# Performance work log

Measured on AMD Instinct MI355X. Metric: run time of the kernel, lower is better.

## Reference

```python
import jax, jax.numpy as jnp
import numpy as np

B, S, DIM, H = 2, 2048, 1024, 16
HD = DIM // H  # 64


def setup_inputs() -> dict:
    key = jax.random.key(0)
    ks = jax.random.split(key, 7)
    sc = 1.0 / np.sqrt(DIM)
    gammas = jnp.asarray(1.0 - 2.0 ** (-5.0 - np.arange(H)), jnp.float32)  # RetNet per-head decay
    return {
        "q": jax.random.normal(ks[0], (B, S, DIM), jnp.float32),
        "k": jax.random.normal(ks[1], (B, S, DIM), jnp.float32),
        "v": jax.random.normal(ks[2], (B, S, DIM), jnp.float32),
        "W_in": jax.random.normal(ks[3], (DIM, DIM), jnp.float32) * sc,
        "b_in": jnp.zeros((DIM,), jnp.float32),
        "W_gate": jax.random.normal(ks[4], (DIM, DIM), jnp.float32) * sc,
        "b_gate": jnp.zeros((DIM,), jnp.float32),
        "W_out": jax.random.normal(ks[5], (DIM, DIM), jnp.float32) * sc,
        "b_out": jnp.zeros((DIM,), jnp.float32),
        "gammas": gammas,
    }


def _mamba(x, W_in, b_in, W_gate, b_gate, W_out, b_out):
    # Gated linear recurrence: h_t = a_t * h_{t-1} + u_t  (selective-scan style)
    u = x @ W_in + b_in          # [B,S,D]
    a = jax.nn.sigmoid(x @ W_gate + b_gate)  # [B,S,D] data-dependent decay gate

    def combine(c1, c2):
        a1, u1 = c1
        a2, u2 = c2
        return (a1 * a2, a2 * u1 + u2)

    _, h = jax.lax.associative_scan(combine, (a, u), axis=1)  # parallel scan over S
    return h @ W_out + b_out  # residual=False, dropout=0.0


def _retention(q, k, v, gammas):
    # Per-head decay-masked attention: out = ((Q K^T / sqrt(hd)) * D) V,
    # D[h,n,m] = gamma_h^(n-m) for n>=m else 0 (causal decay kernel).
    def split(x):
        return x.reshape(B, S, H, HD).transpose(0, 2, 1, 3)  # [B,H,S,HD]

    qh, kh, vh = split(q), split(k), split(v)
    idx = jnp.arange(S)
    diff = idx[:, None] - idx[None, :]                        # [S,S]
    expnt = jnp.maximum(diff, 0).astype(jnp.float32)
    D = jnp.where(diff >= 0, gammas[:, None, None] ** expnt, 0.0)  # [H,S,S]
    scores = jnp.einsum("bhnd,bhmd->bhnm", qh, kh) / np.sqrt(HD)
    out = jnp.einsum("bhnm,bhmd->bhnd", scores * D[None], vh)
    return out.transpose(0, 2, 1, 3).reshape(B, S, DIM)


def reference(q, k, v, W_in, b_in, W_gate, b_gate, W_out, b_out, gammas):
    q_proj = _mamba(q, W_in, b_in, W_gate, b_gate, W_out, b_out)
    return _retention(q_proj, k, v, gammas)
```

## Files before the change

kernel.cpp:

```cpp
#include <hip/hip_runtime.h>
#include <math.h>

#define B_  2
#define S_  2048
#define D_  1024
#define H_  16
#define HD_ 64
#define M_  (B_*S_)

typedef unsigned short ushort_t;
typedef unsigned int   uint_t;
typedef __attribute__((ext_vector_type(8))) short bf16x8;
typedef __attribute__((ext_vector_type(4))) float f32x4;

__device__ __forceinline__ ushort_t f2bf(float f) {
    uint_t u = __builtin_bit_cast(uint_t, f);
    u += 0x7FFFu + ((u >> 16) & 1u);
    return (ushort_t)(u >> 16);
}
__device__ __forceinline__ float bf2f(ushort_t h) {
    uint_t u = (uint_t)h << 16;
    return __builtin_bit_cast(float, u);
}
__device__ __forceinline__ uint_t pkt(float lo, float hi) {
    return __builtin_amdgcn_perm(__builtin_bit_cast(uint_t, hi),
                                 __builtin_bit_cast(uint_t, lo), 0x07060302u);
}
__device__ __forceinline__ void dma16(const ushort_t* g, ushort_t* l) {
    __builtin_amdgcn_global_load_lds(
        (const __attribute__((address_space(1))) uint_t*)g,
        (__attribute__((address_space(3))) uint_t*)l, 16, 0, 0);
}
__device__ __forceinline__ bf16x8 fragr(const ushort_t* base, int row, int chunk) {
    return *(const bf16x8*)&base[row * 64 + (((chunk ^ (row & 7)) << 3))];
}
__device__ __forceinline__ bf16x8 fragr32(const ushort_t* base, int row, int chunk) {
    return *(const bf16x8*)&base[row * 32 + (((chunk ^ ((row >> 1) & 3)) << 3))];
}

__global__ __launch_bounds__(256)
void transp_cvt3(const float* __restrict__ W0, const float* __restrict__ W1,
                 const float* __restrict__ W2, ushort_t* __restrict__ T0,
                 ushort_t* __restrict__ T1, ushort_t* __restrict__ T2) {
    __shared__ float T[32][36];
    const float*  W  = (blockIdx.z == 0) ? W0 : (blockIdx.z == 1) ? W1 : W2;
    ushort_t*     WT = (blockIdx.z == 0) ? T0 : (blockIdx.z == 1) ? T1 : T2;
    const int kt = blockIdx.x, nt = blockIdx.y;
    const int t = threadIdx.x;
    const int rr = t >> 3, cc = (t & 7) * 4;
    float4 w4 = *(const float4*)(W + (size_t)(kt * 32 + rr) * D_ + nt * 32 + cc);
    T[rr][cc + 0] = w4.x; T[rr][cc + 1] = w4.y; T[rr][cc + 2] = w4.z; T[rr][cc + 3] = w4.w;
    __syncthreads();
    ushort_t o[4];
    #pragma unroll
    for (int j = 0; j < 4; ++j) o[j] = f2bf(T[cc + j][rr]);
    *(ushort4*)(WT + (size_t)(nt * 32 + rr) * D_ + kt * 32 + cc) =
        make_ushort4(o[0], o[1], o[2], o[3]);
}

__global__ __launch_bounds__(256)
void cvt_bf16(const float* __restrict__ X, ushort_t* __restrict__ Y) {
    const int i = (blockIdx.x * 256 + threadIdx.x) * 4;
    float4 x = *(const float4*)(X + i);
    *(ushort4*)(Y + i) = make_ushort4(f2bf(x.x), f2bf(x.y), f2bf(x.z), f2bf(x.w));
}

__global__ __launch_bounds__(256)
void kv_cvt_g(const float* __restrict__ K, const float* __restrict__ V,
              const float* __restrict__ gammas, ushort_t* __restrict__ Kb,
              ushort_t* __restrict__ VT, float* __restrict__ Gg) {
    __shared__ ushort_t Tv[64 * 72];
    __shared__ ushort_t Tk[64 * 72];
    const int mt = blockIdx.x, h = blockIdx.y, b = blockIdx.z;
    const int m0 = mt * 64;
    const int tid = threadIdx.x;
    const int r = tid >> 2, c0 = (tid & 3) * 16;
    const float lg = log2f(gammas[h]);
    const float gm = exp2f(-(float)r * lg);
    {
        const float* src = K + ((size_t)(b * S_ + m0 + r)) * D_ + h * HD_ + c0;
        ushort_t kb[16];
        #pragma unroll
        for (int j4 = 0; j4 < 4; ++j4) {
            float4 x = *(const float4*)(src + j4 * 4);
            kb[j4 * 4 + 0] = f2bf(x.x); kb[j4 * 4 + 1] = f2bf(x.y);
            kb[j4 * 4 + 2] = f2bf(x.z); kb[j4 * 4 + 3] = f2bf(x.w);
        }
        ushort_t* dst = Kb + ((size_t)(b * S_ + m0 + r)) * D_ + h * HD_ + c0;
        *(uint4*)(dst + 0) = *(const uint4*)&kb[0];
        *(uint4*)(dst + 8) = *(const uint4*)&kb[8];
        #pragma unroll
        for (int j = 0; j < 16; ++j) Tk[(c0 + j) * 72 + r] = kb[j];
    }
    {
        const float* src = V + ((size_t)(b * S_ + m0 + r)) * D_ + h * HD_ + c0;
        #pragma unroll
        for (int j4 = 0; j4 < 4; ++j4) {
            float4 x = *(const float4*)(src + j4 * 4);
            Tv[(c0 + j4 * 4 + 0) * 72 + r] = f2bf(x.x * gm);
            Tv[(c0 + j4 * 4 + 1) * 72 + r] = f2bf(x.y * gm);
            Tv[(c0 + j4 * 4 + 2) * 72 + r] = f2bf(x.z * gm);
            Tv[(c0 + j4 * 4 + 3) * 72 + r] = f2bf(x.w * gm);
        }
    }
    __syncthreads();
    {
        ushort_t* dst = VT + ((size_t)((b * H_ + h) * HD_ + r)) * S_ + m0 + c0;
        *(uint4*)(dst + 0) = *(const uint4*)&Tv[r * 72 + c0 + 0];
        *(uint4*)(dst + 8) = *(const uint4*)&Tv[r * 72 + c0 + 8];
    }
    const int w = tid >> 6, lane = tid & 63, quad = lane >> 4, l15 = lane & 15;
    bf16x8 af0 = *(const bf16x8*)&Tv[(w * 16 + l15) * 72 + quad * 8];
    bf16x8 af1 = *(const bf16x8*)&Tv[(w * 16 + l15) * 72 + 32 + quad * 8];
    float* gout = Gg + ((size_t)((b * H_ + h) * 32 + mt)) * 4096;
    #pragma unroll
    for (int kt2 = 0; kt2 < 4; ++kt2) {
        bf16x8 bf0 = *(const bf16x8*)&Tk[(kt2 * 16 + l15) * 72 + quad * 8];
        bf16x8 bf1 = *(const bf16x8*)&Tk[(kt2 * 16 + l15) * 72 + 32 + quad * 8];
        f32x4 g = {};
        g = __builtin_amdgcn_mfma_f32_16x16x32_bf16(af0, bf0, g, 0, 0, 0);
        g = __builtin_amdgcn_mfma_f32_16x16x32_bf16(af1, bf1, g, 0, 0, 0);
        #pragma unroll
        for (int reg = 0; reg < 4; ++reg)
            gout[(w * 16 + quad * 4 + reg) * 64 + kt2 * 16 + l15] = g[reg];
    }
}

__global__ __launch_bounds__(256)
void gemm_dual_scan(const ushort_t* __restrict__ A, const ushort_t* __restrict__ BTi,
                    const ushort_t* __restrict__ BTg, const float* __restrict__ bi,
                    const float* __restrict__ bg, float* __restrict__ Hloc,
                    ushort_t* __restrict__ Pp, float* __restrict__ cA,
                    float* __restrict__ cU) {
    __shared__ ushort_t smem[32768];
    const int tid = threadIdx.x;
    const int n0 = blockIdx.x * 64, m0 = blockIdx.y * 128;
    const int w = tid >> 6, lane = tid & 63, quad = lane >> 4, l15 = lane & 15;
    const int wr = (w >> 1) * 64, wc = (w & 1) * 32;
    const int l4 = lane & 3, lr4 = lane >> 2;

    f32x4 acc_i[4][2] = {};
    f32x4 acc_g[4][2] = {};

    auto stage = [&](int k0, int bufo) {
        #pragma unroll
        for (int t = 0; t < 2; ++t) {
            const int row = w * 32 + t * 16 + lr4;
            const int gc = ((l4 ^ ((row >> 1) & 3)) << 3);
            dma16(A + (size_t)(m0 + row) * D_ + k0 + gc, &smem[bufo + row * 32 + l4 * 8]);
        }
        {
            const int row = w * 16 + lr4;
            const int gc = ((l4 ^ ((row >> 1) & 3)) << 3);
            dma16(BTi + (size_t)(n0 + row) * D_ + k0 + gc, &smem[bufo + 4096 + row * 32 + l4 * 8]);
            dma16(BTg + (size_t)(n0 + row) * D_ + k0 + gc, &smem[bufo + 6144 + row * 32 + l4 * 8]);
        }
    };

    stage(0, 0);
    stage(32, 8192);
    stage(64, 16384);
    for (int t = 0; t < 32; ++t) {
        if (t < 30)       asm volatile("s_waitcnt vmcnt(8)" ::: "memory");
        else if (t == 30) asm volatile("s_waitcnt vmcnt(4)" ::: "memory");
        else              asm volatile("s_waitcnt vmcnt(0)" ::: "memory");
        __builtin_amdgcn_s_barrier();
        if (t < 29) stage((t + 3) * 32, ((t + 3) & 3) * 8192);
        const ushort_t* As = smem + (t & 3) * 8192;
        const ushort_t* Bi_ = As + 4096;
        const ushort_t* Bg_ = As + 6144;
        bf16x8 af[4], bfi[2], bfg[2];
        #pragma unroll
        for (int i = 0; i < 4; ++i)
            af[i] = fragr32(As, wr + 16 * i + l15, quad);
        #pragma unroll
        for (int j = 0; j < 2; ++j) {
            bfi[j] = fragr32(Bi_, wc + 16 * j + l15, quad);
            bfg[j] = fragr32(Bg_, wc + 16 * j + l15, quad);
        }
        __builtin_amdgcn_s_setprio(1);
        #pragma unroll
        for (int i = 0; i < 4; ++i)
            #pragma unroll
            for (int j = 0; j < 2; ++j) {
                acc_i[i][j] = __builtin_amdgcn_mfma_f32_16x16x32_bf16(
                    af[i], bfi[j], acc_i[i][j], 0, 0, 0);
                acc_g[i][j] = __builtin_amdgcn_mfma_f32_16x16x32_bf16(
                    af[i], bfg[j], acc_g[i][j], 0, 0, 0);
            }
        __builtin_amdgcn_s_setprio(0);
    }

    ushort_t* Us = smem;
    ushort_t* Gu = smem + 8448;
    #pragma unroll
    for (int j = 0; j < 2; ++j) {
        const int n = wc + 16 * j + l15;
        const float bbi = bi[n0 + n], bbg = bg[n0 + n];
        #pragma unroll
        for (int i = 0; i < 4; ++i) {
            #pragma unroll
            for (int r = 0; r < 4; ++r) {
                const int m = wr + 16 * i + quad * 4 + r;
                Us[m * 66 + n] = f2bf(acc_i[i][j][r] + bbi);
                float g = 1.0f / (1.0f + __expf(-(acc_g[i][j][r] + bbg)));
                Gu[m * 66 + n] = (ushort_t)__float2uint_rn(g * 65535.0f);
            }
        }
    }
    __syncthreads();

    const int nl = tid & 63, c = tid >> 6;
    const int gmb = m0 + c * 32;
    const size_t gbase = (size_t)gmb * D_ + n0 + nl;
    float Aa = 1.0f, hh = 0.0f;
    #pragma unroll 4
    for (int j = 0; j < 32; ++j) {
        const float g = (float)Gu[(c * 32 + j) * 66 + nl] * (1.0f / 65535.0f);
        const float u = bf2f(Us[(c * 32 + j) * 66 + nl]);
        Aa *= g;
        hh = fmaf(g, hh, u);
        Pp[gbase + (size_t)j * D_] = f2bf(Aa);
        Hloc[gbase + (size_t)j * D_] = hh;
    }
    const int bb = gmb >> 11;
    const int ch = (gmb & 2047) >> 5;
    const int ci = ((bb * 64 + ch) << 10) + n0 + nl;
    cA[ci] = Aa;
    cU[ci] = hh;
}

__global__ __launch_bounds__(256)
void mid_scan(const float* __restrict__ Gg, const float* __restrict__ gammas,
              ushort_t* __restrict__ Sb, const float* __restrict__ cA,
              const float* __restrict__ cU, float* __restrict__ cIn) {
    const int bi = blockIdx.x;
    if (bi < 128) {
        const int sl = bi & 3, h = (bi >> 2) & 15, b = bi >> 6;
        const float g64 = exp2f(64.0f * log2f(gammas[h]));
        const int r = threadIdx.x >> 4;
        const int cb = (threadIdx.x & 15) * 4;
        const size_t base = ((size_t)((b * H_ + h) * 32)) * 4096 + (sl * 16 + r) * 64 + cb;
        float4 S = make_float4(0.f, 0.f, 0.f, 0.f);
        for (int c = 0; c < 32; ++c) {
            ushort4 sb;
            sb.x = f2bf(S.x); sb.y = f2bf(S.y); sb.z = f2bf(S.z); sb.w = f2bf(S.w);
            *(ushort4*)(Sb + base + (size_t)c * 4096) = sb;
            float4 G = *(const float4*)(Gg + base + (size_t)c * 4096);
            S.x = g64 * (S.x + G.x); S.y = g64 * (S.y + G.y);
            S.z = g64 * (S.z + G.z); S.w = g64 * (S.w + G.w);
        }
        return;
    }
    const int t = (bi - 128) * 256 + threadIdx.x;
    const int d = t & 1023, b = t >> 10;
    float h = 0.0f;
    for (int c0 = 0; c0 < 64; c0 += 16) {
        float Av[16], Uv[16];
        #pragma unroll
        for (int j = 0; j < 16; ++j) {
            const int idx = ((b * 64 + c0 + j) << 10) + d;
            Av[j] = cA[idx]; Uv[j] = cU[idx];
        }
        #pragma unroll
        for (int j = 0; j < 16; ++j) {
            cIn[((b * 64 + c0 + j) << 10) + d] = h;
            h = fmaf(Av[j], h, Uv[j]);
        }
    }
}

__global__ __launch_bounds__(256)
void scan_fix(const float* __restrict__ Hloc, const ushort_t* __restrict__ Pp,
              const float* __restrict__ cIn, ushort_t* __restrict__ hout) {
    const int i = (blockIdx.x * 256 + threadIdx.x) * 4;
    const int m = i >> 10, d = i & 1023;
    const int b = m >> 11, ch = (m & 2047) >> 5;
    float4 hl = *(const float4*)(Hloc + i);
    ushort4 p4 = *(const ushort4*)(Pp + i);
    float4 ci = *(const float4*)(cIn + ((b * 64 + ch) << 10) + d);
    ushort4 o;
    o.x = f2bf(fmaf(ci.x, bf2f(p4.x), hl.x));
    o.y = f2bf(fmaf(ci.y, bf2f(p4.y), hl.y));
    o.z = f2bf(fmaf(ci.z, bf2f(p4.z), hl.z));
    o.w = f2bf(fmaf(ci.w, bf2f(p4.w), hl.w));
    *(ushort4*)(hout + i) = o;
}

__global__ __launch_bounds__(256)
void gemm_out_a(const ushort_t* __restrict__ A, const ushort_t* __restrict__ BT,
                const float* __restrict__ bias, float scale,
                ushort_t* __restrict__ Cb) {
    __shared__ ushort_t smem[24576];
    const int tid = threadIdx.x;
    const int n0 = blockIdx.x * 64, m0 = blockIdx.y * 128;
    const int w = tid >> 6, lane = tid & 63, quad = lane >> 4, l15 = lane & 15;
    const int wr = (w >> 1) * 64, wc = (w & 1) * 32;
    const int l4 = lane & 3, lr4 = lane >> 2;

    f32x4 acc[4][2] = {};

    auto stage = [&](int k0, int bufo) {
        #pragma unroll
        for (int t = 0; t < 2; ++t) {
            const int row = w * 32 + t * 16 + lr4;
            const int gc = ((l4 ^ ((row >> 1) & 3)) << 3);
            dma16(A + (size_t)(m0 + row) * D_ + k0 + gc, &smem[bufo + row * 32 + l4 * 8]);
        }
        {
            const int row = w * 16 + lr4;
            const int gc = ((l4 ^ ((row >> 1) & 3)) << 3);
            dma16(BT + (size_t)(n0 + row) * D_ + k0 + gc, &smem[bufo + 4096 + row * 32 + l4 * 8]);
        }
    };

    stage(0, 0);
    stage(32, 6144);
    stage(64, 12288);
    for (int t = 0; t < 32; ++t) {
        if (t < 30)       asm volatile("s_waitcnt vmcnt(6)" ::: "memory");
        else if (t == 30) asm volatile("s_waitcnt vmcnt(3)" ::: "memory");
        else              asm volatile("s_waitcnt vmcnt(0)" ::: "memory");
        __builtin_amdgcn_s_barrier();
        if (t < 29) stage((t + 3) * 32, ((t + 3) & 3) * 6144);
        const ushort_t* As = smem + (t & 3) * 6144;
        const ushort_t* Bs = As + 4096;
        bf16x8 af[4], bf[2];
        #pragma unroll
        for (int i = 0; i < 4; ++i)
            af[i] = fragr32(As, wr + 16 * i + l15, quad);
        #pragma unroll
        for (int j = 0; j < 2; ++j)
            bf[j] = fragr32(Bs, wc + 16 * j + l15, quad);
        __builtin_amdgcn_s_setprio(1);
        #pragma unroll
        for (int i = 0; i < 4; ++i)
            #pragma unroll
            for (int j = 0; j < 2; ++j)
                acc[i][j] = __builtin_amdgcn_mfma_f32_16x16x32_bf16(
                    af[i], bf[j], acc[i][j], 0, 0, 0);
        __builtin_amdgcn_s_setprio(0);
    }

    #pragma unroll
    for (int j = 0; j < 2; ++j) {
        const int n = n0 + wc + 16 * j + l15;
        const float bb = bias[n];
        #pragma unroll
        for (int i = 0; i < 4; ++i)
            #pragma unroll
            for (int r = 0; r < 4; ++r) {
                const int m = m0 + wr + 16 * i + quad * 4 + r;
                Cb[(size_t)m * D_ + n] = f2bf((acc[i][j][r] + bb) * scale);
            }
    }
}

__global__ __launch_bounds__(256)
void retention_chunk(const ushort_t* __restrict__ Qb, const ushort_t* __restrict__ Kb,
                     const ushort_t* __restrict__ VT, const ushort_t* __restrict__ Sb,
                     const float* __restrict__ gammas, float* __restrict__ Out) {
    __shared__ ushort_t smem[20480];
    ushort_t* Qs = smem;
    ushort_t* Ks = smem + 4096;
    ushort_t* Vt = smem + 8192;
    ushort_t* Ss = smem + 12288;
    ushort_t* Ps = smem + 16384;
    const int tid = threadIdx.x;
    const int nt = blockIdx.x, h = blockIdx.y, b = blockIdx.z;
    const int n0 = nt * 64;
    const float lg = log2f(gammas[h]);
    const int w = tid >> 6, lane = tid & 63, quad = lane >> 4, l15 = lane & 15;
    const int l8 = lane & 7, lr8 = lane >> 3;
    const int nl = w * 16 + l15;
    const size_t bS = (size_t)b * S_;
    const size_t vrow0 = (size_t)((b * H_ + h) * HD_);
    const size_t sbase = ((size_t)((b * H_ + h) * 32 + nt)) * 4096;

    #pragma unroll
    for (int t = 0; t < 2; ++t) {
        const int row = w * 16 + t * 8 + lr8;
        const int gc = ((l8 ^ (row & 7)) << 3);
        dma16(Qb + (bS + n0 + row) * D_ + h * HD_ + gc, &Qs[row * 64 + l8 * 8]);
        dma16(Kb + (bS + n0 + row) * D_ + h * HD_ + gc, &Ks[row * 64 + l8 * 8]);
        dma16(VT + (vrow0 + row) * S_ + n0 + gc, &Vt[row * 64 + l8 * 8]);
        dma16(Sb + sbase + (size_t)row * 64 + gc, &Ss[row * 64 + l8 * 8]);
    }
    __syncthreads();

    bf16x8 qf0 = fragr(Qs, nl, quad);
    bf16x8 qf1 = fragr(Qs, nl, 4 + quad);

    f32x4 o[4] = {};
    #pragma unroll
    for (int ct = 0; ct < 4; ++ct) {
        bf16x8 sf0 = fragr(Ss, ct * 16 + l15, quad);
        bf16x8 sf1 = fragr(Ss, ct * 16 + l15, 4 + quad);
        o[ct] = __builtin_amdgcn_mfma_f32_16x16x32_bf16(sf0, qf0, o[ct], 0, 0, 0);
        o[ct] = __builtin_amdgcn_mfma_f32_16x16x32_bf16(sf1, qf1, o[ct], 0, 0, 0);
    }
    #pragma unroll
    for (int mt2 = 0; mt2 < 4; ++mt2) {
        bf16x8 kf0 = fragr(Ks, mt2 * 16 + l15, quad);
        bf16x8 kf1 = fragr(Ks, mt2 * 16 + l15, 4 + quad);
        f32x4 s = {};
        s = __builtin_amdgcn_mfma_f32_16x16x32_bf16(kf0, qf0, s, 0, 0, 0);
        s = __builtin_amdgcn_mfma_f32_16x16x32_bf16(kf1, qf1, s, 0, 0, 0);
        const int mbase = mt2 * 16 + quad * 4;
        #pragma unroll
        for (int r = 0; r < 4; ++r)
            if (nl < mbase + r) s[r] = 0.0f;
        uint2 pw; pw.x = pkt(s[0], s[1]); pw.y = pkt(s[2], s[3]);
        const int chunk = mbase >> 3;
        *(uint2*)&Ps[nl * 64 + ((chunk ^ (nl & 7)) << 3) + (mbase & 7)] = pw;
    }
    bf16x8 pf0 = fragr(Ps, nl, quad);
    bf16x8 pf1 = fragr(Ps, nl, 4 + quad);
    #pragma unroll
    for (int ct = 0; ct < 4; ++ct) {
        bf16x8 vf0 = fragr(Vt, ct * 16 + l15, quad);
        bf16x8 vf1 = fragr(Vt, ct * 16 + l15, 4 + quad);
        o[ct] = __builtin_amdgcn_mfma_f32_16x16x32_bf16(vf0, pf0, o[ct], 0, 0, 0);
        o[ct] = __builtin_amdgcn_mfma_f32_16x16x32_bf16(vf1, pf1, o[ct], 0, 0, 0);
    }

    const float esc = exp2f((float)nl * lg);
    const size_t ob = (bS + n0 + nl) * D_ + h * HD_;
    #pragma unroll
    for (int ct = 0; ct < 4; ++ct) {
        f32x4 t = o[ct] * esc;
        *(f32x4*)(Out + ob + ct * 16 + quad * 4) = t;
    }
}

extern "C" void kernel_launch(void* const* d_in, const int* in_sizes, int n_in,
                              void* d_out, int out_size, void* d_ws, size_t ws_size,
                              hipStream_t stream) {
    const float* q      = (const float*)d_in[0];
    const float* k      = (const float*)d_in[1];
    const float* v      = (const float*)d_in[2];
    const float* W_in   = (const float*)d_in[3];
    const float* b_in   = (const float*)d_in[4];
    const float* W_gate = (const float*)d_in[5];
    const float* b_gate = (const float*)d_in[6];
    const float* W_out  = (const float*)d_in[7];
    const float* b_out  = (const float*)d_in[8];
    const float* gammas = (const float*)d_in[9];
    float* out = (float*)d_out;

    char* ws = (char*)d_ws;
    const size_t MB = 1024 * 1024;
    float*    Hloc    = (float*)(ws);
    ushort_t* Pp      = (ushort_t*)(ws + 16 * MB);
    ushort_t* h_bf    = (ushort_t*)(ws + 24 * MB);
    ushort_t* q_bf    = (ushort_t*)(ws + 32 * MB);
    ushort_t* WT_in   = (ushort_t*)(ws + 40 * MB);
    ushort_t* WT_gate = (ushort_t*)(ws + 42 * MB);
    ushort_t* WT_out  = (ushort_t*)(ws + 44 * MB);
    float*    cA      = (float*)(ws + 46 * MB);
    float*    cU      = (float*)(ws + 46 * MB + 512 * 1024);
    float*    cIn     = (float*)(ws + 47 * MB);
    ushort_t* k_bf    = (ushort_t*)(ws + 48 * MB);
    ushort_t* VT      = (ushort_t*)(ws + 56 * MB);
    float*    Gg      = (float*)(ws + 64 * MB);
    ushort_t* Sb      = (ushort_t*)(ws + 80 * MB);
    ushort_t* qp_bf   = q_bf;

    transp_cvt3<<<dim3(D_ / 32, D_ / 32, 3), 256, 0, stream>>>(
        W_in, W_gate, W_out, WT_in, WT_gate, WT_out);
    cvt_bf16<<<(M_ * D_) / (256 * 4), 256, 0, stream>>>(q, q_bf);

    gemm_dual_scan<<<dim3(D_ / 64, M_ / 128), 256, 0, stream>>>(
        q_bf, WT_in, WT_gate, b_in, b_gate, Hloc, Pp, cA, cU);

    kv_cvt_g<<<dim3(S_ / 64, H_, B_), 256, 0, stream>>>(k, v, gammas, k_bf, VT, Gg);

    mid_scan<<<136, 256, 0, stream>>>(Gg, gammas, Sb, cA, cU, cIn);
    scan_fix<<<(M_ * D_) / 1024, 256, 0, stream>>>(Hloc, Pp, cIn, h_bf);

    gemm_out_a<<<dim3(D_ / 64, M_ / 128), 256, 0, stream>>>(
        h_bf, WT_out, b_out, 0.125f, qp_bf);

    retention_chunk<<<dim3(S_ / 64, H_, B_), 256, 0, stream>>>(
        qp_bf, k_bf, VT, Sb, gammas, out);
}
```

Baseline: 192.4 us.

## Switch projection GEMMs to double-buffered LDS pipeline with higher occupancy bound

Replaces the 4-stage LDS ring with manual vmcnt waits in the dual-scan and output GEMMs with a simple 2-buffer ping-pong synchronized by __syncthreads, halving shared memory per block. It also adds a launch-bounds minimum of 4 blocks per CU and drops the s_setprio hints. The aim is more resident blocks to hide latency instead of deep prefetching within one block. In exchange it gives up the deeper pipeline and adds a full barrier each iteration, which may expose global load latency.

```diff
diff --git a/kernel.cpp b/kernel.cpp
--- a/kernel.cpp
+++ b/kernel.cpp
@@ -126,13 +126,13 @@
     }
 }
 
-__global__ __launch_bounds__(256)
+__global__ __launch_bounds__(256, 4)
 void gemm_dual_scan(const ushort_t* __restrict__ A, const ushort_t* __restrict__ BTi,
                     const ushort_t* __restrict__ BTg, const float* __restrict__ bi,
                     const float* __restrict__ bg, float* __restrict__ Hloc,
                     ushort_t* __restrict__ Pp, float* __restrict__ cA,
                     float* __restrict__ cU) {
-    __shared__ ushort_t smem[32768];
+    __shared__ ushort_t smem[16896];
     const int tid = threadIdx.x;
     const int n0 = blockIdx.x * 64, m0 = blockIdx.y * 128;
     const int w = tid >> 6, lane = tid & 63, quad = lane >> 4, l15 = lane & 15;
@@ -158,15 +158,11 @@
     };
 
     stage(0, 0);
-    stage(32, 8192);
-    stage(64, 16384);
+    __syncthreads();
     for (int t = 0; t < 32; ++t) {
-        if (t < 30)       asm volatile("s_waitcnt vmcnt(8)" ::: "memory");
-        else if (t == 30) asm volatile("s_waitcnt vmcnt(4)" ::: "memory");
-        else              asm volatile("s_waitcnt vmcnt(0)" ::: "memory");
-        __builtin_amdgcn_s_barrier();
-        if (t < 29) stage((t + 3) * 32, ((t + 3) & 3) * 8192);
-        const ushort_t* As = smem + (t & 3) * 8192;
+        const int bufo = (t & 1) * 8192;
+        if (t < 31) stage((t + 1) * 32, 8192 - bufo);
+        const ushort_t* As = smem + bufo;
         const ushort_t* Bi_ = As + 4096;
         const ushort_t* Bg_ = As + 6144;
         bf16x8 af[4], bfi[2], bfg[2];
@@ -178,7 +174,6 @@
             bfi[j] = fragr32(Bi_, wc + 16 * j + l15, quad);
             bfg[j] = fragr32(Bg_, wc + 16 * j + l15, quad);
         }
-        __builtin_amdgcn_s_setprio(1);
         #pragma unroll
         for (int i = 0; i < 4; ++i)
             #pragma unroll
@@ -188,7 +183,7 @@
                 acc_g[i][j] = __builtin_amdgcn_mfma_f32_16x16x32_bf16(
                     af[i], bfg[j], acc_g[i][j], 0, 0, 0);
             }
-        __builtin_amdgcn_s_setprio(0);
+        __syncthreads();
     }
 
     ushort_t* Us = smem;
@@ -287,11 +282,11 @@
     *(ushort4*)(hout + i) = o;
 }
 
-__global__ __launch_bounds__(256)
+__global__ __launch_bounds__(256, 4)
 void gemm_out_a(const ushort_t* __restrict__ A, const ushort_t* __restrict__ BT,
                 const float* __restrict__ bias, float scale,
                 ushort_t* __restrict__ Cb) {
-    __shared__ ushort_t smem[24576];
+    __shared__ ushort_t smem[12288];
     const int tid = threadIdx.x;
     const int n0 = blockIdx.x * 64, m0 = blockIdx.y * 128;
     const int w = tid >> 6, lane = tid & 63, quad = lane >> 4, l15 = lane & 15;
@@ -315,15 +310,11 @@
     };
 
     stage(0, 0);
-    stage(32, 6144);
-    stage(64, 12288);
+    __syncthreads();
     for (int t = 0; t < 32; ++t) {
-        if (t < 30)       asm volatile("s_waitcnt vmcnt(6)" ::: "memory");
-        else if (t == 30) asm volatile("s_waitcnt vmcnt(3)" ::: "memory");
-        else              asm volatile("s_waitcnt vmcnt(0)" ::: "memory");
-        __builtin_amdgcn_s_barrier();
-        if (t < 29) stage((t + 3) * 32, ((t + 3) & 3) * 6144);
-        const ushort_t* As = smem + (t & 3) * 6144;
+        const int bufo = (t & 1) * 6144;
+        if (t < 31) stage((t + 1) * 32, 6144 - bufo);
+        const ushort_t* As = smem + bufo;
         const ushort_t* Bs = As + 4096;
         bf16x8 af[4], bf[2];
         #pragma unroll
@@ -332,14 +323,13 @@
         #pragma unroll
         for (int j = 0; j < 2; ++j)
             bf[j] = fragr32(Bs, wc + 16 * j + l15, quad);
-        __builtin_amdgcn_s_setprio(1);
         #pragma unroll
         for (int i = 0; i < 4; ++i)
             #pragma unroll
             for (int j = 0; j < 2; ++j)
                 acc[i][j] = __builtin_amdgcn_mfma_f32_16x16x32_bf16(
                     af[i], bf[j], acc[i][j], 0, 0, 0);
-        __builtin_amdgcn_s_setprio(0);
+        __syncthreads();
     }
 
     #pragma unroll
```

Result: no change. 190.6 us (-1.0%).
